# Kernel optimization log

Hardware: AMD Instinct MI355X
Metric: run time of the kernel (lower is better)

Reference implementation:

```python
import jax, jax.numpy as jnp
import numpy as np

NUM_CLASSES = 80
NUM_ATTRIB = 5 + NUM_CLASSES  # 85
STRIDES = [32, 16, 8]
BASE_SIZES = [
    [(116, 90), (156, 198), (373, 326)],
    [(30, 61), (62, 45), (59, 119)],
    [(10, 13), (16, 30), (33, 23)],
]


def _grid_anchors(H, W, stride, base_sizes):
    # YOLOAnchorGenerator: base anchors centered at (stride/2, stride/2),
    # shifted by x*stride, y*stride over the grid. Anchor-major layout to
    # match the head's (N, A, H, W, attrib) flatten order.
    ws = jnp.array([b[0] for b in base_sizes], jnp.float32)
    hs = jnp.array([b[1] for b in base_sizes], jnp.float32)
    c = 0.5 * stride
    base = jnp.stack([c - 0.5 * ws, c - 0.5 * hs, c + 0.5 * ws, c + 0.5 * hs], axis=-1)  # [A,4]
    xs = jnp.arange(W, dtype=jnp.float32) * stride
    ys = jnp.arange(H, dtype=jnp.float32) * stride
    sx, sy = jnp.meshgrid(xs, ys)  # [H,W] each
    shifts = jnp.stack([sx, sy, sx, sy], axis=-1).reshape(-1, 4)  # [H*W,4]
    return (base[:, None, :] + shifts[None, :, :]).reshape(-1, 4)  # [A*H*W,4]


def _bbox_decode(anchors, pred, stride):
    # Faithful to YOLOXHead_yzf._bbox_decode with train=True (tlbr output).
    cx = (anchors[..., 0] + anchors[..., 2]) * 0.5
    cy = (anchors[..., 1] + anchors[..., 3]) * 0.5
    wa = anchors[..., 2] - anchors[..., 0]
    ha = anchors[..., 3] - anchors[..., 1]
    xc = (pred[..., 0] - 0.5) * stride + cx
    yc = (pred[..., 1] - 0.5) * stride + cy
    w = jnp.exp(pred[..., 2]) * wa
    h = jnp.exp(pred[..., 3]) * ha
    return jnp.stack([xc - 0.5 * w, yc - 0.5 * h, xc + 0.5 * w, yc + 0.5 * h], axis=-1)


def _forward(pred_maps):
    outs = []
    for lvl, pm in enumerate(pred_maps):
        N, _, H, W = pm.shape
        A = len(BASE_SIZES[lvl])
        # (N, A*attrib, H, W) -> (N, A, H, W, attrib) -> (N, A*H*W, attrib)
        p = pm.reshape(N, A, NUM_ATTRIB, H, W).transpose(0, 1, 3, 4, 2).reshape(N, -1, NUM_ATTRIB)
        anchors = _grid_anchors(H, W, STRIDES[lvl], BASE_SIZES[lvl])  # [A*H*W,4]
        boxes = _bbox_decode(anchors, p[..., :4], STRIDES[lvl])
        obj = jax.nn.sigmoid(p[..., 4:5])
        cls = jax.nn.sigmoid(p[..., 5:])
        outs.append(jnp.concatenate([boxes, obj, cls], axis=-1))
    return jnp.concatenate(outs, axis=1)  # (N, 25200, 85)


def setup_inputs() -> dict:
    key = jax.random.key(0)
    k0, k1, k2 = jax.random.split(key, 3)
    scale = 0.1  # keep exp(pred_wh) well-behaved
    return {
        "pred_map_0": jax.random.normal(k0, (32, 255, 20, 20), jnp.float32) * scale,
        "pred_map_1": jax.random.normal(k1, (32, 255, 40, 40), jnp.float32) * scale,
        "pred_map_2": jax.random.normal(k2, (32, 255, 80, 80), jnp.float32) * scale,
    }


def reference(pred_map_0, pred_map_1, pred_map_2):
    return _forward([pred_map_0, pred_map_1, pred_map_2])
```

## Files before the change

### kernel.cpp

```cpp
#include <hip/hip_runtime.h>


typedef float v4f __attribute__((ext_vector_type(4)));

#define NATT 85
#define TP 64
#define TOTAL_ROWS 25200
#define NIT 6

__device__ __forceinline__ float sigmf(float v) {
    return 1.0f / (1.0f + __expf(-v));
}

template <int LVL>
__device__ __forceinline__ void process(const float* __restrict__ in,
                                        float* __restrict__ out,
                                        int id, float* lds) {
    constexpr int   H  = (LVL == 0) ? 20 : (LVL == 1) ? 40 : 80;
    constexpr int   W  = H;
    constexpr int   HW = H * W;
    constexpr float S  = (LVL == 0) ? 32.f : (LVL == 1) ? 16.f : 8.f;
    constexpr int   OUT_BASE = (LVL == 0) ? 0 : (LVL == 1) ? 1200 : 6000;
    constexpr int   C  = (HW + TP - 1) / TP;

    const int tid   = threadIdx.x;
    const int chunk = id % C;
    const int ta    = id / C;
    const int a     = ta % 3;
    const int n     = ta / 3;

    const int pos0  = chunk * TP;
    const int valid = (HW - pos0 < TP) ? (HW - pos0) : TP;

    const float* inp = in + ((size_t)n * 255 + (size_t)a * NATT) * HW + pos0;

    const int m  = tid & 15;
    const int p  = m * 4;
    const int k0 = tid >> 4;
    const bool act = (p < valid);

    v4f r[NIT];
#pragma unroll
    for (int it = 0; it < NIT; ++it) {
        const int kk = k0 + it * 16;
        if (kk < NATT && act) {
            r[it] = *reinterpret_cast<const v4f*>(inp + (size_t)kk * HW + p);
        }
    }
#pragma unroll
    for (int it = 0; it < NIT; ++it) {
        const int kk = k0 + it * 16;
        if (kk < NATT && act) {
            v4f v = r[it];
            if (kk >= 4) {
                v.x = sigmf(v.x); v.y = sigmf(v.y);
                v.z = sigmf(v.z); v.w = sigmf(v.w);
            }
            lds[(p + 0) * NATT + kk] = v.x;
            lds[(p + 1) * NATT + kk] = v.y;
            lds[(p + 2) * NATT + kk] = v.z;
            lds[(p + 3) * NATT + kk] = v.w;
        }
    }
    __syncthreads();

    if (tid < TP && tid < valid) {
        const int gp = pos0 + tid;
        const int y  = gp / W;
        const int x  = gp - y * W;
        const float wa = (a == 0) ? ((LVL == 0) ? 116.f : (LVL == 1) ? 30.f : 10.f)
                       : (a == 1) ? ((LVL == 0) ? 156.f : (LVL == 1) ? 62.f : 16.f)
                                  : ((LVL == 0) ? 373.f : (LVL == 1) ? 59.f : 33.f);
        const float ha = (a == 0) ? ((LVL == 0) ?  90.f : (LVL == 1) ? 61.f : 13.f)
                       : (a == 1) ? ((LVL == 0) ? 198.f : (LVL == 1) ? 45.f : 30.f)
                                  : ((LVL == 0) ? 326.f : (LVL == 1) ? 119.f : 23.f);
        const float p0 = lds[tid * NATT + 0];
        const float p1 = lds[tid * NATT + 1];
        const float p2 = lds[tid * NATT + 2];
        const float p3 = lds[tid * NATT + 3];
        const float xc = (p0 + (float)x) * S;
        const float yc = (p1 + (float)y) * S;
        const float w  = __expf(p2) * wa;
        const float h  = __expf(p3) * ha;
        lds[tid * NATT + 0] = xc - 0.5f * w;
        lds[tid * NATT + 1] = yc - 0.5f * h;
        lds[tid * NATT + 2] = xc + 0.5f * w;
        lds[tid * NATT + 3] = yc + 0.5f * h;
    }
    __syncthreads();

    const size_t row0 = (size_t)n * TOTAL_ROWS + OUT_BASE + (size_t)a * HW + pos0;
    float* op = out + row0 * NATT;
    const int nfl = valid * NATT;
    for (int i = tid * 4; i + 3 < nfl; i += 1024) {
        __builtin_nontemporal_store(*reinterpret_cast<const v4f*>(lds + i),
                                    reinterpret_cast<v4f*>(op + i));
    }
}

__global__ __launch_bounds__(256) void yolox_fused(const float* __restrict__ in0,
                                                   const float* __restrict__ in1,
                                                   const float* __restrict__ in2,
                                                   float* __restrict__ out) {
    __shared__ float lds[TP * NATT];
    const int bid = blockIdx.x;
    if (bid < 9600) {
        process<2>(in2, out, bid, lds);
    } else if (bid < 12000) {
        process<1>(in1, out, bid - 9600, lds);
    } else {
        process<0>(in0, out, bid - 12000, lds);
    }
}

extern "C" void kernel_launch(void* const* d_in, const int* in_sizes, int n_in,
                              void* d_out, int out_size, void* d_ws, size_t ws_size,
                              hipStream_t stream) {
    const float* in0 = (const float*)d_in[0];
    const float* in1 = (const float*)d_in[1];
    const float* in2 = (const float*)d_in[2];
    float* out = (float*)d_out;

    yolox_fused<<<dim3(12672), dim3(256), 0, stream>>>(in0, in1, in2, out);
}
```

Baseline: 92.27 us.

## Process two tiles per block with overlapped loads and fused box decode via shuffles

Each block now handles two consecutive tiles. The second tile's global loads are issued before the first tile's output stores, so memory reads and writes overlap, and the grid is halved. Box decoding is folded into the scatter phase: lanes exchange the xy and wh predictions with a cross-lane shuffle, which removes one LDS round-trip and one barrier per tile. This raises register pressure (two register sets) and reduces the number of blocks, which may hurt latency hiding.

Result: slower. 96.27 us (+4.3%).

```diff
diff --git a/kernel.cpp b/kernel.cpp
--- a/kernel.cpp
+++ b/kernel.cpp
@@ -12,90 +12,150 @@
     return 1.0f / (1.0f + __expf(-v));
 }
 
+template <int LVL> struct G {
+    static constexpr int   H  = (LVL == 0) ? 20 : (LVL == 1) ? 40 : 80;
+    static constexpr int   W  = H;
+    static constexpr int   HW = H * W;
+    static constexpr float S  = (LVL == 0) ? 32.f : (LVL == 1) ? 16.f : 8.f;
+    static constexpr int   OUT_BASE = (LVL == 0) ? 0 : (LVL == 1) ? 1200 : 6000;
+    static constexpr int   C  = (HW + TP - 1) / TP;
+};
+
+struct Tile {
+    const float* inp;
+    int pos0, valid, a, n;
+};
+
 template <int LVL>
-__device__ __forceinline__ void process(const float* __restrict__ in,
-                                        float* __restrict__ out,
-                                        int id, float* lds) {
-    constexpr int   H  = (LVL == 0) ? 20 : (LVL == 1) ? 40 : 80;
-    constexpr int   W  = H;
-    constexpr int   HW = H * W;
-    constexpr float S  = (LVL == 0) ? 32.f : (LVL == 1) ? 16.f : 8.f;
-    constexpr int   OUT_BASE = (LVL == 0) ? 0 : (LVL == 1) ? 1200 : 6000;
-    constexpr int   C  = (HW + TP - 1) / TP;
+__device__ __forceinline__ Tile mk_tile(const float* __restrict__ in, int id) {
+    Tile t;
+    const int chunk = id % G<LVL>::C;
+    const int ta    = id / G<LVL>::C;
+    t.a     = ta % 3;
+    t.n     = ta / 3;
+    t.pos0  = chunk * TP;
+    const int rem = G<LVL>::HW - t.pos0;
+    t.valid = rem < TP ? rem : TP;
+    t.inp   = in + ((size_t)t.n * 255 + (size_t)t.a * NATT) * G<LVL>::HW + t.pos0;
+    return t;
+}
 
-    const int tid   = threadIdx.x;
-    const int chunk = id % C;
-    const int ta    = id / C;
-    const int a     = ta % 3;
-    const int n     = ta / 3;
-
-    const int pos0  = chunk * TP;
-    const int valid = (HW - pos0 < TP) ? (HW - pos0) : TP;
-
-    const float* inp = in + ((size_t)n * 255 + (size_t)a * NATT) * HW + pos0;
-
-    const int m  = tid & 15;
-    const int p  = m * 4;
+template <int LVL>
+__device__ __forceinline__ void issue(const Tile& t, v4f r[NIT], int tid) {
+    const int p  = (tid & 15) * 4;
     const int k0 = tid >> 4;
-    const bool act = (p < valid);
-
-    v4f r[NIT];
 #pragma unroll
-    for (int it = 0; it < NIT; ++it) {
-        const int kk = k0 + it * 16;
-        if (kk < NATT && act) {
-            r[it] = *reinterpret_cast<const v4f*>(inp + (size_t)kk * HW + p);
+    for (int it = 0; it < NIT; ++it) r[it] = v4f{0.f, 0.f, 0.f, 0.f};
+    if (p < t.valid) {
+#pragma unroll
+        for (int it = 0; it < NIT; ++it) {
+            const int kk = k0 + it * 16;
+            if (kk < NATT)
+                r[it] = *reinterpret_cast<const v4f*>(t.inp + (size_t)kk * G<LVL>::HW + p);
         }
     }
-#pragma unroll
-    for (int it = 0; it < NIT; ++it) {
-        const int kk = k0 + it * 16;
-        if (kk < NATT && act) {
-            v4f v = r[it];
-            if (kk >= 4) {
-                v.x = sigmf(v.x); v.y = sigmf(v.y);
-                v.z = sigmf(v.z); v.w = sigmf(v.w);
-            }
-            lds[(p + 0) * NATT + kk] = v.x;
-            lds[(p + 1) * NATT + kk] = v.y;
-            lds[(p + 2) * NATT + kk] = v.z;
-            lds[(p + 3) * NATT + kk] = v.w;
-        }
-    }
-    __syncthreads();
+}
 
-    if (tid < TP && tid < valid) {
-        const int gp = pos0 + tid;
-        const int y  = gp / W;
-        const int x  = gp - y * W;
+template <int LVL>
+__device__ __forceinline__ void scatter(const Tile& t, v4f r[NIT], float* lds, int tid) {
+    const int m   = tid & 15;
+    const int p   = m * 4;
+    const int k0  = tid >> 4;
+    const bool act = (p < t.valid);
+
+    if (tid < 64) {
+        v4f mine = r[0];
+        v4f part;
+        part.x = __shfl_xor(mine.x, 32);
+        part.y = __shfl_xor(mine.y, 32);
+        part.z = __shfl_xor(mine.z, 32);
+        part.w = __shfl_xor(mine.w, 32);
+
+        const int a = t.a;
         const float wa = (a == 0) ? ((LVL == 0) ? 116.f : (LVL == 1) ? 30.f : 10.f)
                        : (a == 1) ? ((LVL == 0) ? 156.f : (LVL == 1) ? 62.f : 16.f)
                                   : ((LVL == 0) ? 373.f : (LVL == 1) ? 59.f : 33.f);
         const float ha = (a == 0) ? ((LVL == 0) ?  90.f : (LVL == 1) ? 61.f : 13.f)
                        : (a == 1) ? ((LVL == 0) ? 198.f : (LVL == 1) ? 45.f : 30.f)
                                   : ((LVL == 0) ? 326.f : (LVL == 1) ? 119.f : 23.f);
-        const float p0 = lds[tid * NATT + 0];
-        const float p1 = lds[tid * NATT + 1];
-        const float p2 = lds[tid * NATT + 2];
-        const float p3 = lds[tid * NATT + 3];
-        const float xc = (p0 + (float)x) * S;
-        const float yc = (p1 + (float)y) * S;
-        const float w  = __expf(p2) * wa;
-        const float h  = __expf(p3) * ha;
-        lds[tid * NATT + 0] = xc - 0.5f * w;
-        lds[tid * NATT + 1] = yc - 0.5f * h;
-        lds[tid * NATT + 2] = xc + 0.5f * w;
-        lds[tid * NATT + 3] = yc + 0.5f * h;
+        const float dim = (k0 & 1) ? ha : wa;
+        const float sgn = (k0 & 2) ? 0.5f : -0.5f;
+
+        if (act) {
+#pragma unroll
+            for (int j = 0; j < 4; ++j) {
+                const int gp = t.pos0 + p + j;
+                const int y  = gp / G<LVL>::W;
+                const int x  = gp - y * G<LVL>::W;
+                const float coord = (k0 & 1) ? (float)y : (float)x;
+                const float pc = (k0 & 2) ? part[j] : mine[j];
+                const float pe = (k0 & 2) ? mine[j] : part[j];
+                const float c  = (pc + coord) * G<LVL>::S;
+                const float e  = __expf(pe) * dim;
+                lds[(p + j) * NATT + k0] = c + sgn * e;
+            }
+#pragma unroll
+            for (int it = 1; it < NIT; ++it) {
+                const int kk = k0 + it * 16;
+                v4f v = r[it];
+                v.x = sigmf(v.x); v.y = sigmf(v.y);
+                v.z = sigmf(v.z); v.w = sigmf(v.w);
+                lds[(p + 0) * NATT + kk] = v.x;
+                lds[(p + 1) * NATT + kk] = v.y;
+                lds[(p + 2) * NATT + kk] = v.z;
+                lds[(p + 3) * NATT + kk] = v.w;
+            }
+        }
+    } else {
+        if (act) {
+#pragma unroll
+            for (int it = 0; it < NIT; ++it) {
+                const int kk = k0 + it * 16;
+                if (kk < NATT) {
+                    v4f v = r[it];
+                    v.x = sigmf(v.x); v.y = sigmf(v.y);
+                    v.z = sigmf(v.z); v.w = sigmf(v.w);
+                    lds[(p + 0) * NATT + kk] = v.x;
+                    lds[(p + 1) * NATT + kk] = v.y;
+                    lds[(p + 2) * NATT + kk] = v.z;
+                    lds[(p + 3) * NATT + kk] = v.w;
+                }
+            }
+        }
     }
-    __syncthreads();
+}
 
-    const size_t row0 = (size_t)n * TOTAL_ROWS + OUT_BASE + (size_t)a * HW + pos0;
+template <int LVL>
+__device__ __forceinline__ void write_out(const Tile& t, const float* lds,
+                                          float* __restrict__ out, int tid) {
+    const size_t row0 = (size_t)t.n * TOTAL_ROWS + G<LVL>::OUT_BASE
+                      + (size_t)t.a * G<LVL>::HW + t.pos0;
     float* op = out + row0 * NATT;
-    const int nfl = valid * NATT;
+    const int nfl = t.valid * NATT;
     for (int i = tid * 4; i + 3 < nfl; i += 1024) {
         __builtin_nontemporal_store(*reinterpret_cast<const v4f*>(lds + i),
                                     reinterpret_cast<v4f*>(op + i));
     }
+}
+
+template <int LVL>
+__device__ __forceinline__ void process2(const float* __restrict__ in,
+                                         float* __restrict__ out,
+                                         int pair, float* lds) {
+    const int tid = threadIdx.x;
+    const Tile t0 = mk_tile<LVL>(in, 2 * pair);
+    const Tile t1 = mk_tile<LVL>(in, 2 * pair + 1);
+    v4f r0[NIT], r1[NIT];
+
+    issue<LVL>(t0, r0, tid);
+    scatter<LVL>(t0, r0, lds, tid);
+    __syncthreads();
+    issue<LVL>(t1, r1, tid);
+    write_out<LVL>(t0, lds, out, tid);
+    __syncthreads();
+    scatter<LVL>(t1, r1, lds, tid);
+    __syncthreads();
+    write_out<LVL>(t1, lds, out, tid);
 }
 
 __global__ __launch_bounds__(256) void yolox_fused(const float* __restrict__ in0,
@@ -104,12 +164,12 @@
                                                    float* __restrict__ out) {
     __shared__ float lds[TP * NATT];
     const int bid = blockIdx.x;
-    if (bid < 9600) {
-        process<2>(in2, out, bid, lds);
-    } else if (bid < 12000) {
-        process<1>(in1, out, bid - 9600, lds);
+    if (bid < 4800) {
+        process2<2>(in2, out, bid, lds);
+    } else if (bid < 6000) {
+        process2<1>(in1, out, bid - 4800, lds);
     } else {
-        process<0>(in0, out, bid - 12000, lds);
+        process2<0>(in0, out, bid - 6000, lds);
     }
 }
 
@@ -121,5 +181,5 @@
     const float* in2 = (const float*)d_in[2];
     float* out = (float*)d_out;
 
-    yolox_fused<<<dim3(12672), dim3(256), 0, stream>>>(in0, in1, in2, out);
+    yolox_fused<<<dim3(6336), dim3(256), 0, stream>>>(in0, in1, in2, out);
 }
```
